# Optimization experiments

Hardware: AMD Instinct MI355X
Metric: run time of the kernel (lower is better)

## Reference

```python
import jax, jax.numpy as jnp
import numpy as np

B, LS, LW, D = 4, 160, 128, 768
POS_DIM = WD = PWD = DDD = 64
MAX_SPAN = 8
NZ = int(LW * 0.5)          # span_pruned_threshold = 0.5
HID = 128
SPAN_DIM = 2 * D + 2 * POS_DIM + WD      # 1728
PAIR_DIM = 2 * SPAN_DIM + PWD + DDD      # 3584
BINS = np.array([0, 1, 2, 3, 4, 5, 6, 7, 8, 9, 10, 15, 20, 25, 30, 50, 80])

def _span_indices(n, max_span):
    # enumeration order matches the torch loop: window = 1..max_span, start ascending
    s, e = [], []
    for w in range(1, min(n, max_span) + 1):
        st = np.arange(n - w + 1)
        s.append(st); e.append(st + w - 1)
    return np.concatenate(s), np.concatenate(e)

STARTS, ENDS = _span_indices(LW, MAX_SPAN)   # [S], S = 996
NUM_SPANS = len(STARTS)
WIDTH_IDS = np.searchsorted(BINS, ENDS - STARTS + 1, side='right') - 1  # bucket_embedding


def setup_inputs() -> dict:
    key = jax.random.key(0)
    ks = jax.random.split(key, 20)
    w = lambda k, shape, s=0.05: (jax.random.normal(k, shape, dtype=jnp.float32) * s)
    return {
        "last_hidden": jax.random.normal(ks[0], (B, LS, D), dtype=jnp.float32),
        "bert_subword_mask_matrix": jax.random.uniform(ks[1], (B, LS, LS), dtype=jnp.float32),
        "word_len": jnp.ones((B, LW), dtype=jnp.float32),
        "pos_table": w(ks[2], (50, POS_DIM), 1.0),
        "width_table": w(ks[3], (17, WD), 1.0),
        "rel_table": w(ks[4], (17, PWD), 1.0),
        "dep_table": w(ks[5], (30, DDD), 1.0),
        "sW1": w(ks[6], (SPAN_DIM, HID)), "sb1": jnp.zeros((HID,), jnp.float32),
        "sW2": w(ks[7], (HID, HID)),      "sb2": jnp.zeros((HID,), jnp.float32),
        "sW3": w(ks[8], (HID, 3)),        "sb3": jnp.zeros((3,), jnp.float32),
        "pW1": w(ks[9], (PAIR_DIM, HID)), "pb1": jnp.zeros((HID,), jnp.float32),
        "pW2": w(ks[10], (HID, HID)),     "pb2": jnp.zeros((HID,), jnp.float32),
        "pW3": w(ks[11], (HID, 4)),       "pb3": jnp.zeros((4,), jnp.float32),
        "first_subword_seq": jnp.sort(jax.random.randint(ks[12], (B, LW), 0, LS), axis=-1),
        "pos_id": jax.random.randint(ks[13], (B, LW), 0, 50),
        "dep_dis": jax.random.randint(ks[14], (B, LW, LW), 0, 30),
    }


def _ffnn(x, W1, b1, W2, b2, W3, b3):
    h = jax.nn.relu(x @ W1 + b1)
    h = jax.nn.relu(h @ W2 + b2)
    return h @ W3 + b3          # dropout is identity in eval mode


def reference(last_hidden, bert_subword_mask_matrix, word_len,
              pos_table, width_table, rel_table, dep_table,
              sW1, sb1, sW2, sb2, sW3, sb3,
              pW1, pb1, pW2, pb2, pW3, pb3,
              first_subword_seq, pos_id, dep_dis):
    # subword -> word features
    feats = jnp.einsum('bst,btd->bsd', bert_subword_mask_matrix, last_hidden)   # [B,LS,D]
    feats = jnp.take_along_axis(feats, first_subword_seq[:, :, None], axis=1)   # [B,LW,D]
    feats = feats / word_len[:, :, None]
    pos_feats = pos_table[pos_id]                                               # [B,LW,64]

    # span representation: [x_i; x_j; p_i; p_j; width_emb]
    w_emb = width_table[WIDTH_IDS]                                              # [S,64]
    spans = jnp.concatenate([
        feats[:, STARTS], feats[:, ENDS],
        pos_feats[:, STARTS], pos_feats[:, ENDS],
        jnp.broadcast_to(w_emb[None], (B, NUM_SPANS, WD))], axis=-1)            # [B,S,1728]

    span_prob = _ffnn(spans, sW1, sb1, sW2, sb2, sW3, sb3)                       # [B,S,3]

    # pruned target/opinion spans
    t_idx = jax.lax.top_k(span_prob[:, :, 1], NZ)[1]                             # [B,NZ]
    o_idx = jax.lax.top_k(span_prob[:, :, 2], NZ)[1]
    t_pair = jnp.repeat(t_idx, NZ, axis=1)                                       # itertools.product order
    o_pair = jnp.tile(o_idx, (1, NZ))                                            # [B,P], P = NZ*NZ

    starts = jnp.asarray(STARTS); ends = jnp.asarray(ENDS)
    a, b = starts[t_pair], ends[t_pair]
    c, d = starts[o_pair], ends[o_pair]

    # f_distance: min(|b-c|, |a-d|), bucketed
    rel = jnp.minimum(jnp.abs(b - c), jnp.abs(a - d))
    rel_ids = jnp.searchsorted(jnp.asarray(BINS), rel, side='right') - 1
    rel_emb = rel_table[rel_ids]                                                 # [B,P,64]

    # dep distance: min of dep_dis[a:b+1, c:d+1]
    BIG = jnp.int32(2 ** 30)
    dep_pad = jnp.pad(dep_dis.astype(jnp.int32),
                      ((0, 0), (0, MAX_SPAN), (0, MAX_SPAN)), constant_values=2 ** 30)
    r = jnp.arange(MAX_SPAN)

    def block_min(dm, ai, bi, ci, di):
        blk = jax.lax.dynamic_slice(dm, (ai, ci), (MAX_SPAN, MAX_SPAN))
        mask = (r[:, None] <= bi - ai) & (r[None, :] <= di - ci)
        return jnp.min(jnp.where(mask, blk, BIG))

    dep_ids = jax.vmap(jax.vmap(block_min, in_axes=(None, 0, 0, 0, 0)),
                       in_axes=(0, 0, 0, 0, 0))(dep_pad, a, b, c, d)             # [B,P]
    dep_emb = dep_table[dep_ids]                                                 # [B,P,64]

    span_t = jnp.take_along_axis(spans, t_pair[:, :, None], axis=1)              # [B,P,1728]
    span_o = jnp.take_along_axis(spans, o_pair[:, :, None], axis=1)
    pair_feat = jnp.concatenate([span_t, span_o, rel_emb, dep_emb], axis=-1)     # [B,P,3584]

    pair_prob = _ffnn(pair_feat, pW1, pb1, pW2, pb2, pW3, pb3)                   # [B,P,4]
    return span_prob, pair_prob
```

## Files before the change

### kernel.cpp

```cpp
#include <hip/hip_runtime.h>

#define BB 4
#define LS 160
#define LW 128
#define DD 768
#define NSPANS 996
#define NZv 64
#define NPAIR 4096
#define HID 128
#define XLD 832
#define PROJ_N 393216


__device__ inline void span_decode(int s, int& st, int& en, int& w) {
  int ww = 1, base = 0;
  while (ww < 8 && s >= base + (129 - ww)) { base += 129 - ww; ++ww; }
  st = s - base; en = st + ww - 1; w = ww;
}

__device__ inline int bucket17(int v) {
  const int BINSv[17] = {0,1,2,3,4,5,6,7,8,9,10,15,20,25,30,50,80};
  int r = 0;
#pragma unroll
  for (int k = 1; k < 17; ++k) r += (v >= BINSv[k]) ? 1 : 0;
  return r;
}

__global__ __launch_bounds__(256) void prep_kernel(
    const float* __restrict__ mask, const float* __restrict__ lh,
    const int* __restrict__ fss, const float* __restrict__ wlen,
    const int* __restrict__ pos_id, const float* __restrict__ pos_table,
    const float* __restrict__ width_table, const float* __restrict__ rel_table,
    const float* __restrict__ dep_table, const float* __restrict__ sW1,
    const float* __restrict__ pW1, const float* __restrict__ sb1,
    const float* __restrict__ pb1, float* __restrict__ X,
    float* __restrict__ tabs) {
  int gid = blockIdx.x;
  int tid = threadIdx.x;
  if (gid < 96) {
    int nt = gid % 12, mt = gid / 12;
    int b = mt >> 1;
    int row0 = mt * 64, c0 = nt * 64;
    __shared__ float as[16][68];
    __shared__ float bs[16][68];
    __shared__ int fssl[64];
    __shared__ float wll[64];
    if (tid < 64) { fssl[tid] = fss[row0 + tid]; wll[tid] = wlen[row0 + tid]; }
    __syncthreads();
    int rg = tid >> 4, tc = tid & 15;
    float acc[4][4] = {{0.f}};
    for (int k0 = 0; k0 < LS; k0 += 16) {
      {
        int r = tid >> 2, kb = (tid & 3) * 4;
        float4 mv = *(const float4*)(mask + (size_t)(b * LS + fssl[r]) * LS + k0 + kb);
        as[kb + 0][r] = mv.x; as[kb + 1][r] = mv.y;
        as[kb + 2][r] = mv.z; as[kb + 3][r] = mv.w;
      }
      {
        int c = tid & 63, kq = tid >> 6;
#pragma unroll
        for (int q = 0; q < 4; ++q) {
          int kk = kq * 4 + q;
          bs[kk][c] = lh[(size_t)(b * LS + k0 + kk) * DD + c0 + c];
        }
      }
      __syncthreads();
#pragma unroll
      for (int kk = 0; kk < 16; ++kk) {
        float av[4], bv[4];
#pragma unroll
        for (int i = 0; i < 4; ++i) av[i] = as[kk][rg * 4 + i];
#pragma unroll
        for (int j = 0; j < 4; ++j) bv[j] = bs[kk][tc * 4 + j];
#pragma unroll
        for (int i = 0; i < 4; ++i)
#pragma unroll
          for (int j = 0; j < 4; ++j) acc[i][j] += av[i] * bv[j];
      }
      __syncthreads();
    }
#pragma unroll
    for (int i = 0; i < 4; ++i) {
      int r = rg * 4 + i;
      float wl = wll[r];
      float4 v = make_float4(acc[i][0] / wl, acc[i][1] / wl, acc[i][2] / wl, acc[i][3] / wl);
      *(float4*)(X + (size_t)(row0 + r) * XLD + c0 + tc * 4) = v;
    }
  } else if (gid < 104) {
    int e0 = (gid - 96) * 4096 + tid * 16;
    int row = e0 >> 6, c0 = e0 & 63;
    const float* src = pos_table + pos_id[row] * 64 + c0;
    float* dst = X + (size_t)row * XLD + 768 + c0;
#pragma unroll
    for (int q = 0; q < 4; ++q)
      *(float4*)(dst + q * 4) = *(const float4*)(src + q * 4);
  } else {
    int bt = gid - 104;
    const float *src, *W, *bias; int rows; float* out;
    switch (bt) {
      case 0: src = width_table; W = sW1 + 1664 * HID; bias = sb1;    rows = 17; out = tabs;        break;
      case 1: src = width_table; W = pW1 + 1664 * HID; bias = nullptr; rows = 17; out = tabs + 2176; break;
      case 2: src = width_table; W = pW1 + 3392 * HID; bias = nullptr; rows = 17; out = tabs + 4352; break;
      case 3: src = rel_table;   W = pW1 + 3456 * HID; bias = nullptr; rows = 17; out = tabs + 6528; break;
      default:src = dep_table;   W = pW1 + 3520 * HID; bias = pb1;    rows = 30; out = tabs + 8704; break;
    }
    for (int e = tid; e < rows * HID; e += 256) {
      int r = e >> 7, c = e & 127;
      float acc = 0.f;
#pragma unroll 8
      for (int k = 0; k < 64; ++k) acc += src[r * 64 + k] * W[k * HID + c];
      out[e] = acc + (bias ? bias[c] : 0.f);
    }
  }
}

__global__ __launch_bounds__(256) void proj_gemm(
    const float* __restrict__ X, const float* __restrict__ sW1,
    const float* __restrict__ pW1, float* __restrict__ part) {
  int nt = blockIdx.x, mt = blockIdx.y, ks = blockIdx.z;
  const int f_offs[6] = {0, 768, 0, 768, 1728, 2496};
  const int p_offs[6] = {1536, 1600, 1536, 1600, 3264, 3328};
  int g = nt >> 1;
  const float* Wb = (g < 2) ? sW1 : pW1;
  int f_off = f_offs[g], p_off = p_offs[g];
  int c0 = (nt & 1) * 64;
  int row0 = mt * 64;
  int kbase = ks * 416;
  __shared__ float as[16][68];
  __shared__ float bs[16][68];
  int tid = threadIdx.x;
  int rg = tid >> 4, tc = tid & 15;
  float acc[4][4] = {{0.f}};
  for (int k0 = 0; k0 < 416; k0 += 16) {
    {
      int r = tid >> 2, kb = (tid & 3) * 4;
      float4 xv = *(const float4*)(X + (size_t)(row0 + r) * XLD + kbase + k0 + kb);
      as[kb + 0][r] = xv.x; as[kb + 1][r] = xv.y;
      as[kb + 2][r] = xv.z; as[kb + 3][r] = xv.w;
    }
    {
      int c = tid & 63, kq = tid >> 6;
#pragma unroll
      for (int q = 0; q < 4; ++q) {
        int kk = kq * 4 + q;
        int kg = kbase + k0 + kk;
        int wr = (kg < 768) ? (f_off + kg) : (p_off + kg - 768);
        bs[kk][c] = Wb[(size_t)wr * HID + c0 + c];
      }
    }
    __syncthreads();
#pragma unroll
    for (int kk = 0; kk < 16; ++kk) {
      float av[4], bv[4];
#pragma unroll
      for (int i = 0; i < 4; ++i) av[i] = as[kk][rg * 4 + i];
#pragma unroll
      for (int j = 0; j < 4; ++j) bv[j] = bs[kk][tc * 4 + j];
#pragma unroll
      for (int i = 0; i < 4; ++i)
#pragma unroll
        for (int j = 0; j < 4; ++j) acc[i][j] += av[i] * bv[j];
    }
    __syncthreads();
  }
#pragma unroll
  for (int i = 0; i < 4; ++i) {
    int row = row0 + rg * 4 + i;
    int bb = row >> 7, iloc = row & 127;
    float* dst = part + (size_t)ks * PROJ_N +
                 ((size_t)(g * BB + bb) * LW + iloc) * HID + c0 + tc * 4;
    *(float4*)dst = make_float4(acc[i][0], acc[i][1], acc[i][2], acc[i][3]);
  }
}

__global__ __launch_bounds__(256) void span_kernel(
    const float* __restrict__ part, const float* __restrict__ tabs,
    const float* __restrict__ sW2, const float* __restrict__ sb2,
    const float* __restrict__ sW3, const float* __restrict__ sb3,
    float* __restrict__ out) {
  int b = blockIdx.y, s0 = blockIdx.x * 32;
  int cnt = min(32, NSPANS - s0);
  __shared__ float h[32][129];
  __shared__ float wsh[16][132];
  __shared__ int stl[32], enl[32], wdl[32];
  int tid = threadIdx.x;
  if (tid < 32 && tid < cnt) {
    int st, en, w; span_decode(s0 + tid, st, en, w);
    stl[tid] = st; enl[tid] = en; wdl[tid] = w;
  }
  __syncthreads();
  const float* SA0 = part + (size_t)(0 * BB + b) * LW * HID;
  const float* SB0 = part + (size_t)(1 * BB + b) * LW * HID;
  const float* SA1 = SA0 + PROJ_N;
  const float* SB1 = SB0 + PROJ_N;
  const float* SW = tabs;
#pragma unroll
  for (int u = 0; u < 16; ++u) {
    int e = tid + u * 256; int r = e >> 7, c = e & 127;
    float v = 0.f;
    if (r < cnt) {
      int sa = stl[r] * HID + c, sb = enl[r] * HID + c;
      v = ((SA0[sa] + SA1[sa]) + (SB0[sb] + SB1[sb])) + SW[wdl[r] * HID + c];
    }
    h[r][c] = fmaxf(v, 0.f);
  }
  __syncthreads();
  int rg = tid >> 5, tc = tid & 31;
  float acc[4][4] = {{0.f}};
  for (int k0 = 0; k0 < HID; k0 += 16) {
#pragma unroll
    for (int u = 0; u < 8; ++u) {
      int idx = tid + u * 256; int r = idx >> 7, c = idx & 127;
      wsh[r][c] = sW2[(k0 + r) * HID + c];
    }
    __syncthreads();
#pragma unroll
    for (int kk = 0; kk < 16; ++kk) {
      float av[4], bv[4];
#pragma unroll
      for (int i = 0; i < 4; ++i) av[i] = h[rg * 4 + i][k0 + kk];
#pragma unroll
      for (int j = 0; j < 4; ++j) bv[j] = wsh[kk][tc * 4 + j];
#pragma unroll
      for (int i = 0; i < 4; ++i)
#pragma unroll
        for (int j = 0; j < 4; ++j) acc[i][j] += av[i] * bv[j];
    }
    __syncthreads();
  }
  __shared__ float h2[32][129];
#pragma unroll
  for (int i = 0; i < 4; ++i)
#pragma unroll
    for (int j = 0; j < 4; ++j)
      h2[rg * 4 + i][tc * 4 + j] = fmaxf(acc[i][j] + sb2[tc * 4 + j], 0.f);
  __syncthreads();
  if (tid < 96) {
    int sl = tid / 3, oc = tid - sl * 3;
    if (sl < cnt) {
      float a = sb3[oc];
#pragma unroll 16
      for (int k = 0; k < HID; ++k) a += h2[sl][k] * sW3[k * 3 + oc];
      out[(b * NSPANS + s0 + sl) * 3 + oc] = a;
    }
  }
}

__global__ __launch_bounds__(256) void topk_kernel(
    const float* __restrict__ out, int* __restrict__ tix, int* __restrict__ oix) {
  int b = blockIdx.y, ch = blockIdx.x + 1;
  __shared__ unsigned long long keys[1024];
  int tid = threadIdx.x;
#pragma unroll
  for (int u = 0; u < 4; ++u) {
    int e = tid + u * 256;
    unsigned long long kk = 0ull;
    if (e < NSPANS) {
      unsigned int bits = __float_as_uint(out[(b * NSPANS + e) * 3 + ch]);
      unsigned int mv = (bits & 0x80000000u) ? ~bits : (bits | 0x80000000u);
      kk = ((unsigned long long)mv << 32) | (unsigned long long)(0xFFFFFFFFu - e);
    }
    keys[e] = kk;
  }
  __syncthreads();
  for (int k = 2; k <= 1024; k <<= 1) {
    for (int j = k >> 1; j > 0; j >>= 1) {
#pragma unroll
      for (int u = 0; u < 4; ++u) {
        int i = tid + u * 256;
        int l = i ^ j;
        if (l > i) {
          unsigned long long a = keys[i], c = keys[l];
          bool desc = ((i & k) == 0);
          if (desc ? (a < c) : (a > c)) { keys[i] = c; keys[l] = a; }
        }
      }
      __syncthreads();
    }
  }
  int* dst = (ch == 1 ? tix : oix) + b * NZv;
  if (tid < NZv) dst[tid] = (int)(0xFFFFFFFFu - (unsigned int)keys[tid]);
}

__global__ __launch_bounds__(256) void pair_kernel(
    const float* __restrict__ part, const float* __restrict__ tabs,
    const int* __restrict__ tix, const int* __restrict__ oix,
    const int* __restrict__ dep_dis, const float* __restrict__ pW2,
    const float* __restrict__ pb2, const float* __restrict__ pW3,
    const float* __restrict__ pb3, float* __restrict__ out) {
  int b = blockIdx.y, p0 = blockIdx.x * 64;
  __shared__ float h[64][129];
  __shared__ float wsh[16][132];
  __shared__ int mTA[64], mTB[64], mOA[64], mOB[64], mTW[64], mOW[64], mR[64], mD[64];
  int tid = threadIdx.x;
  {
    int m = tid >> 2, sub = tid & 3;
    int p = p0 + m;
    int ti = tix[b * NZv + (p >> 6)];
    int oi = oix[b * NZv + (p & 63)];
    int a, bb2, wt, c, d, wo;
    span_decode(ti, a, bb2, wt);
    span_decode(oi, c, d, wo);
    int mn = 0x7FFFFFFF;
    const int* dp = dep_dis + b * LW * LW;
    for (int x = a; x <= bb2; ++x)
      for (int y = c + sub; y <= d; y += 4)
        mn = min(mn, dp[x * LW + y]);
    mn = min(mn, __shfl_xor(mn, 1));
    mn = min(mn, __shfl_xor(mn, 2));
    if (sub == 0) {
      int rel = min(abs(bb2 - c), abs(a - d));
      mTA[m] = ((2 * BB + b) * LW + a)   * HID;
      mTB[m] = ((3 * BB + b) * LW + bb2) * HID;
      mOA[m] = ((4 * BB + b) * LW + c)   * HID;
      mOB[m] = ((5 * BB + b) * LW + d)   * HID;
      mTW[m] = 2176 + wt * HID;
      mOW[m] = 4352 + wo * HID;
      mR[m]  = 6528 + bucket17(rel) * HID;
      mD[m]  = 8704 + mn * HID;
    }
  }
  __syncthreads();
#pragma unroll
  for (int u = 0; u < 32; ++u) {
    int e = tid + u * 256; int r = e >> 7, c = e & 127;
    int ta = mTA[r] + c, tb = mTB[r] + c, oa = mOA[r] + c, ob = mOB[r] + c;
    float v = (part[ta] + part[ta + PROJ_N]) + (part[tb] + part[tb + PROJ_N]) +
              (part[oa] + part[oa + PROJ_N]) + (part[ob] + part[ob + PROJ_N]) +
              tabs[mTW[r] + c] + tabs[mOW[r] + c] +
              tabs[mR[r] + c] + tabs[mD[r] + c];
    h[r][c] = fmaxf(v, 0.f);
  }
  __syncthreads();
  int tr = tid >> 5, tc = tid & 31;
  float acc[8][4] = {{0.f}};
  for (int k0 = 0; k0 < HID; k0 += 16) {
#pragma unroll
    for (int u = 0; u < 8; ++u) {
      int idx = tid + u * 256; int r = idx >> 7, c = idx & 127;
      wsh[r][c] = pW2[(k0 + r) * HID + c];
    }
    __syncthreads();
#pragma unroll
    for (int kk = 0; kk < 16; ++kk) {
      float av[8], bv[4];
#pragma unroll
      for (int i = 0; i < 8; ++i) av[i] = h[tr + 8 * i][k0 + kk];
#pragma unroll
      for (int j = 0; j < 4; ++j) bv[j] = wsh[kk][tc + 32 * j];
#pragma unroll
      for (int i = 0; i < 8; ++i)
#pragma unroll
        for (int j = 0; j < 4; ++j) acc[i][j] += av[i] * bv[j];
    }
    __syncthreads();
  }
#pragma unroll
  for (int i = 0; i < 8; ++i)
#pragma unroll
    for (int j = 0; j < 4; ++j)
      h[tr + 8 * i][tc + 32 * j] = fmaxf(acc[i][j] + pb2[tc + 32 * j], 0.f);
  __syncthreads();
  {
    int sl = tid >> 2, oc = tid & 3;
    float a = pb3[oc];
#pragma unroll 16
    for (int k = 0; k < HID; ++k) a += h[sl][k] * pW3[k * 4 + oc];
    out[BB * NSPANS * 3 + (b * NPAIR + p0 + sl) * 4 + oc] = a;
  }
}

extern "C" void kernel_launch(void* const* d_in, const int* in_sizes, int n_in,
                              void* d_out, int out_size, void* d_ws, size_t ws_size,
                              hipStream_t stream) {
  const float* last_hidden = (const float*)d_in[0];
  const float* mask        = (const float*)d_in[1];
  const float* word_len    = (const float*)d_in[2];
  const float* pos_table   = (const float*)d_in[3];
  const float* width_table = (const float*)d_in[4];
  const float* rel_table   = (const float*)d_in[5];
  const float* dep_table   = (const float*)d_in[6];
  const float* sW1 = (const float*)d_in[7];
  const float* sb1 = (const float*)d_in[8];
  const float* sW2 = (const float*)d_in[9];
  const float* sb2 = (const float*)d_in[10];
  const float* sW3 = (const float*)d_in[11];
  const float* sb3 = (const float*)d_in[12];
  const float* pW1 = (const float*)d_in[13];
  const float* pb1 = (const float*)d_in[14];
  const float* pW2 = (const float*)d_in[15];
  const float* pb2 = (const float*)d_in[16];
  const float* pW3 = (const float*)d_in[17];
  const float* pb3 = (const float*)d_in[18];
  const int* fss     = (const int*)d_in[19];
  const int* pos_id  = (const int*)d_in[20];
  const int* dep_dis = (const int*)d_in[21];

  float* ws   = (float*)d_ws;
  float* X    = ws;
  float* part = ws + 425984;
  float* tabs = ws + 1212416;
  int*   tix  = (int*)(ws + 1224960);
  int*   oix  = tix + 256;
  float* out  = (float*)d_out;

  prep_kernel<<<109, 256, 0, stream>>>(mask, last_hidden, fss, word_len,
                                       pos_id, pos_table, width_table, rel_table,
                                       dep_table, sW1, pW1, sb1, pb1, X, tabs);
  proj_gemm<<<dim3(12, 8, 2), 256, 0, stream>>>(X, sW1, pW1, part);
  span_kernel<<<dim3(32, BB), 256, 0, stream>>>(part, tabs, sW2, sb2, sW3, sb3, out);
  topk_kernel<<<dim3(2, BB), 256, 0, stream>>>(out, tix, oix);
  pair_kernel<<<dim3(64, BB), 256, 0, stream>>>(part, tabs, tix, oix, dep_dis,
                                                pW2, pb2, pW3, pb3, out);
}
```

Measured before the change: 222.1 us.

## Fuse five stage kernels into one cooperative persistent kernel with grid syncs

Merges prep, projection GEMM, span FFNN, top-k and pair FFNN into a single cooperative kernel of 256 blocks. Stages are separated by grid.sync() and share one union of shared-memory layouts. This removes four kernel launches and the gaps between them. In exchange, shared memory per block grows to the size of the largest stage, many blocks sit idle in the small stages, and each grid barrier has its own cost.

```diff
diff --git a/kernel.cpp b/kernel.cpp
--- a/kernel.cpp
+++ b/kernel.cpp
@@ -1,4 +1,7 @@
 #include <hip/hip_runtime.h>
+#include <hip/hip_cooperative_groups.h>
+
+namespace cg = cooperative_groups;
 
 #define BB 4
 #define LS 160
@@ -26,42 +29,56 @@
   return r;
 }
 
-__global__ __launch_bounds__(256) void prep_kernel(
+struct FeatsSM { float as[16][68]; float bs[16][68]; int fssl[64]; float wll[64]; };
+struct ProjSM  { float as[16][68]; float bs[16][68]; };
+struct SpanSM  { float h[32][129]; float h2[32][129]; float wsh[16][132];
+                 int stl[32], enl[32], wdl[32]; };
+struct TopkSM  { unsigned long long keys[1024]; };
+struct PairSM  { float h[64][129]; float wsh[16][132];
+                 int mTA[64], mTB[64], mOA[64], mOB[64],
+                     mTW[64], mOW[64], mR[64], mD[64]; };
+union AllSM { FeatsSM f; ProjSM p; SpanSM s; TopkSM t; PairSM q; };
+
+__global__ __launch_bounds__(256) void fused_kernel(
     const float* __restrict__ mask, const float* __restrict__ lh,
     const int* __restrict__ fss, const float* __restrict__ wlen,
     const int* __restrict__ pos_id, const float* __restrict__ pos_table,
     const float* __restrict__ width_table, const float* __restrict__ rel_table,
-    const float* __restrict__ dep_table, const float* __restrict__ sW1,
-    const float* __restrict__ pW1, const float* __restrict__ sb1,
-    const float* __restrict__ pb1, float* __restrict__ X,
-    float* __restrict__ tabs) {
-  int gid = blockIdx.x;
-  int tid = threadIdx.x;
+    const float* __restrict__ dep_table,
+    const float* __restrict__ sW1, const float* __restrict__ sb1,
+    const float* __restrict__ sW2, const float* __restrict__ sb2,
+    const float* __restrict__ sW3, const float* __restrict__ sb3,
+    const float* __restrict__ pW1, const float* __restrict__ pb1,
+    const float* __restrict__ pW2, const float* __restrict__ pb2,
+    const float* __restrict__ pW3, const float* __restrict__ pb3,
+    const int* __restrict__ dep_dis,
+    float* __restrict__ X, float* __restrict__ part, float* __restrict__ tabs,
+    int* __restrict__ tix, int* __restrict__ oix, float* __restrict__ out) {
+  cg::grid_group grid = cg::this_grid();
+  int gid = blockIdx.x, tid = threadIdx.x;
+  __shared__ __align__(16) AllSM sm;
+
   if (gid < 96) {
     int nt = gid % 12, mt = gid / 12;
     int b = mt >> 1;
     int row0 = mt * 64, c0 = nt * 64;
-    __shared__ float as[16][68];
-    __shared__ float bs[16][68];
-    __shared__ int fssl[64];
-    __shared__ float wll[64];
-    if (tid < 64) { fssl[tid] = fss[row0 + tid]; wll[tid] = wlen[row0 + tid]; }
+    if (tid < 64) { sm.f.fssl[tid] = fss[row0 + tid]; sm.f.wll[tid] = wlen[row0 + tid]; }
     __syncthreads();
     int rg = tid >> 4, tc = tid & 15;
     float acc[4][4] = {{0.f}};
     for (int k0 = 0; k0 < LS; k0 += 16) {
       {
         int r = tid >> 2, kb = (tid & 3) * 4;
-        float4 mv = *(const float4*)(mask + (size_t)(b * LS + fssl[r]) * LS + k0 + kb);
-        as[kb + 0][r] = mv.x; as[kb + 1][r] = mv.y;
-        as[kb + 2][r] = mv.z; as[kb + 3][r] = mv.w;
+        float4 mv = *(const float4*)(mask + (size_t)(b * LS + sm.f.fssl[r]) * LS + k0 + kb);
+        sm.f.as[kb + 0][r] = mv.x; sm.f.as[kb + 1][r] = mv.y;
+        sm.f.as[kb + 2][r] = mv.z; sm.f.as[kb + 3][r] = mv.w;
       }
       {
         int c = tid & 63, kq = tid >> 6;
 #pragma unroll
         for (int q = 0; q < 4; ++q) {
           int kk = kq * 4 + q;
-          bs[kk][c] = lh[(size_t)(b * LS + k0 + kk) * DD + c0 + c];
+          sm.f.bs[kk][c] = lh[(size_t)(b * LS + k0 + kk) * DD + c0 + c];
         }
       }
       __syncthreads();
@@ -69,9 +86,9 @@
       for (int kk = 0; kk < 16; ++kk) {
         float av[4], bv[4];
 #pragma unroll
-        for (int i = 0; i < 4; ++i) av[i] = as[kk][rg * 4 + i];
-#pragma unroll
-        for (int j = 0; j < 4; ++j) bv[j] = bs[kk][tc * 4 + j];
+        for (int i = 0; i < 4; ++i) av[i] = sm.f.as[kk][rg * 4 + i];
+#pragma unroll
+        for (int j = 0; j < 4; ++j) bv[j] = sm.f.bs[kk][tc * 4 + j];
 #pragma unroll
         for (int i = 0; i < 4; ++i)
 #pragma unroll
@@ -82,7 +99,7 @@
 #pragma unroll
     for (int i = 0; i < 4; ++i) {
       int r = rg * 4 + i;
-      float wl = wll[r];
+      float wl = sm.f.wll[r];
       float4 v = make_float4(acc[i][0] / wl, acc[i][1] / wl, acc[i][2] / wl, acc[i][3] / wl);
       *(float4*)(X + (size_t)(row0 + r) * XLD + c0 + tc * 4) = v;
     }
@@ -94,292 +111,271 @@
 #pragma unroll
     for (int q = 0; q < 4; ++q)
       *(float4*)(dst + q * 4) = *(const float4*)(src + q * 4);
-  } else {
+  } else if (gid < 109) {
     int bt = gid - 104;
-    const float *src, *W, *bias; int rows; float* out;
+    const float *src, *W, *bias; int rows; float* o;
     switch (bt) {
-      case 0: src = width_table; W = sW1 + 1664 * HID; bias = sb1;    rows = 17; out = tabs;        break;
-      case 1: src = width_table; W = pW1 + 1664 * HID; bias = nullptr; rows = 17; out = tabs + 2176; break;
-      case 2: src = width_table; W = pW1 + 3392 * HID; bias = nullptr; rows = 17; out = tabs + 4352; break;
-      case 3: src = rel_table;   W = pW1 + 3456 * HID; bias = nullptr; rows = 17; out = tabs + 6528; break;
-      default:src = dep_table;   W = pW1 + 3520 * HID; bias = pb1;    rows = 30; out = tabs + 8704; break;
+      case 0: src = width_table; W = sW1 + 1664 * HID; bias = sb1;    rows = 17; o = tabs;        break;
+      case 1: src = width_table; W = pW1 + 1664 * HID; bias = nullptr; rows = 17; o = tabs + 2176; break;
+      case 2: src = width_table; W = pW1 + 3392 * HID; bias = nullptr; rows = 17; o = tabs + 4352; break;
+      case 3: src = rel_table;   W = pW1 + 3456 * HID; bias = nullptr; rows = 17; o = tabs + 6528; break;
+      default:src = dep_table;   W = pW1 + 3520 * HID; bias = pb1;    rows = 30; o = tabs + 8704; break;
     }
     for (int e = tid; e < rows * HID; e += 256) {
       int r = e >> 7, c = e & 127;
       float acc = 0.f;
 #pragma unroll 8
       for (int k = 0; k < 64; ++k) acc += src[r * 64 + k] * W[k * HID + c];
-      out[e] = acc + (bias ? bias[c] : 0.f);
+      o[e] = acc + (bias ? bias[c] : 0.f);
     }
   }
-}
-
-__global__ __launch_bounds__(256) void proj_gemm(
-    const float* __restrict__ X, const float* __restrict__ sW1,
-    const float* __restrict__ pW1, float* __restrict__ part) {
-  int nt = blockIdx.x, mt = blockIdx.y, ks = blockIdx.z;
-  const int f_offs[6] = {0, 768, 0, 768, 1728, 2496};
-  const int p_offs[6] = {1536, 1600, 1536, 1600, 3264, 3328};
-  int g = nt >> 1;
-  const float* Wb = (g < 2) ? sW1 : pW1;
-  int f_off = f_offs[g], p_off = p_offs[g];
-  int c0 = (nt & 1) * 64;
-  int row0 = mt * 64;
-  int kbase = ks * 416;
-  __shared__ float as[16][68];
-  __shared__ float bs[16][68];
-  int tid = threadIdx.x;
-  int rg = tid >> 4, tc = tid & 15;
-  float acc[4][4] = {{0.f}};
-  for (int k0 = 0; k0 < 416; k0 += 16) {
+  grid.sync();
+
+  if (gid < 192) {
+    int nt = gid % 12, mt = (gid / 12) % 8, ks = gid / 96;
+    const int f_offs[6] = {0, 768, 0, 768, 1728, 2496};
+    const int p_offs[6] = {1536, 1600, 1536, 1600, 3264, 3328};
+    int g = nt >> 1;
+    const float* Wb = (g < 2) ? sW1 : pW1;
+    int f_off = f_offs[g], p_off = p_offs[g];
+    int c0 = (nt & 1) * 64;
+    int row0 = mt * 64;
+    int kbase = ks * 416;
+    int rg = tid >> 4, tc = tid & 15;
+    float acc[4][4] = {{0.f}};
+    for (int k0 = 0; k0 < 416; k0 += 16) {
+      {
+        int r = tid >> 2, kb = (tid & 3) * 4;
+        float4 xv = *(const float4*)(X + (size_t)(row0 + r) * XLD + kbase + k0 + kb);
+        sm.p.as[kb + 0][r] = xv.x; sm.p.as[kb + 1][r] = xv.y;
+        sm.p.as[kb + 2][r] = xv.z; sm.p.as[kb + 3][r] = xv.w;
+      }
+      {
+        int c = tid & 63, kq = tid >> 6;
+#pragma unroll
+        for (int q = 0; q < 4; ++q) {
+          int kk = kq * 4 + q;
+          int kg = kbase + k0 + kk;
+          int wr = (kg < 768) ? (f_off + kg) : (p_off + kg - 768);
+          sm.p.bs[kk][c] = Wb[(size_t)wr * HID + c0 + c];
+        }
+      }
+      __syncthreads();
+#pragma unroll
+      for (int kk = 0; kk < 16; ++kk) {
+        float av[4], bv[4];
+#pragma unroll
+        for (int i = 0; i < 4; ++i) av[i] = sm.p.as[kk][rg * 4 + i];
+#pragma unroll
+        for (int j = 0; j < 4; ++j) bv[j] = sm.p.bs[kk][tc * 4 + j];
+#pragma unroll
+        for (int i = 0; i < 4; ++i)
+#pragma unroll
+          for (int j = 0; j < 4; ++j) acc[i][j] += av[i] * bv[j];
+      }
+      __syncthreads();
+    }
+#pragma unroll
+    for (int i = 0; i < 4; ++i) {
+      int row = row0 + rg * 4 + i;
+      int bb = row >> 7, iloc = row & 127;
+      float* dst = part + (size_t)ks * PROJ_N +
+                   ((size_t)(g * BB + bb) * LW + iloc) * HID + c0 + tc * 4;
+      *(float4*)dst = make_float4(acc[i][0], acc[i][1], acc[i][2], acc[i][3]);
+    }
+  }
+  grid.sync();
+
+  if (gid < 128) {
+    int b = gid >> 5, s0 = (gid & 31) * 32;
+    int cnt = min(32, NSPANS - s0);
+    if (tid < 32 && tid < cnt) {
+      int st, en, w; span_decode(s0 + tid, st, en, w);
+      sm.s.stl[tid] = st; sm.s.enl[tid] = en; sm.s.wdl[tid] = w;
+    }
+    __syncthreads();
+    const float* SA0 = part + (size_t)(0 * BB + b) * LW * HID;
+    const float* SB0 = part + (size_t)(1 * BB + b) * LW * HID;
+    const float* SA1 = SA0 + PROJ_N;
+    const float* SB1 = SB0 + PROJ_N;
+    const float* SW = tabs;
+#pragma unroll
+    for (int u = 0; u < 16; ++u) {
+      int e = tid + u * 256; int r = e >> 7, c = e & 127;
+      float v = 0.f;
+      if (r < cnt) {
+        int sa = sm.s.stl[r] * HID + c, sb = sm.s.enl[r] * HID + c;
+        v = ((SA0[sa] + SA1[sa]) + (SB0[sb] + SB1[sb])) + SW[sm.s.wdl[r] * HID + c];
+      }
+      sm.s.h[r][c] = fmaxf(v, 0.f);
+    }
+    __syncthreads();
+    int rg = tid >> 5, tc = tid & 31;
+    float acc[4][4] = {{0.f}};
+    for (int k0 = 0; k0 < HID; k0 += 16) {
+#pragma unroll
+      for (int u = 0; u < 8; ++u) {
+        int idx = tid + u * 256; int r = idx >> 7, c = idx & 127;
+        sm.s.wsh[r][c] = sW2[(k0 + r) * HID + c];
+      }
+      __syncthreads();
+#pragma unroll
+      for (int kk = 0; kk < 16; ++kk) {
+        float av[4], bv[4];
+#pragma unroll
+        for (int i = 0; i < 4; ++i) av[i] = sm.s.h[rg * 4 + i][k0 + kk];
+#pragma unroll
+        for (int j = 0; j < 4; ++j) bv[j] = sm.s.wsh[kk][tc * 4 + j];
+#pragma unroll
+        for (int i = 0; i < 4; ++i)
+#pragma unroll
+          for (int j = 0; j < 4; ++j) acc[i][j] += av[i] * bv[j];
+      }
+      __syncthreads();
+    }
+#pragma unroll
+    for (int i = 0; i < 4; ++i)
+#pragma unroll
+      for (int j = 0; j < 4; ++j)
+        sm.s.h2[rg * 4 + i][tc * 4 + j] = fmaxf(acc[i][j] + sb2[tc * 4 + j], 0.f);
+    __syncthreads();
+    if (tid < 96) {
+      int sl = tid / 3, oc = tid - sl * 3;
+      if (sl < cnt) {
+        float a = sb3[oc];
+#pragma unroll 16
+        for (int k = 0; k < HID; ++k) a += sm.s.h2[sl][k] * sW3[k * 3 + oc];
+        out[(b * NSPANS + s0 + sl) * 3 + oc] = a;
+      }
+    }
+  }
+  grid.sync();
+
+  if (gid < 8) {
+    int b = gid >> 1, ch = (gid & 1) + 1;
+#pragma unroll
+    for (int u = 0; u < 4; ++u) {
+      int e = tid + u * 256;
+      unsigned long long kk = 0ull;
+      if (e < NSPANS) {
+        unsigned int bits = __float_as_uint(out[(b * NSPANS + e) * 3 + ch]);
+        unsigned int mv = (bits & 0x80000000u) ? ~bits : (bits | 0x80000000u);
+        kk = ((unsigned long long)mv << 32) | (unsigned long long)(0xFFFFFFFFu - e);
+      }
+      sm.t.keys[e] = kk;
+    }
+    __syncthreads();
+    for (int k = 2; k <= 1024; k <<= 1) {
+      for (int j = k >> 1; j > 0; j >>= 1) {
+#pragma unroll
+        for (int u = 0; u < 4; ++u) {
+          int i = tid + u * 256;
+          int l = i ^ j;
+          if (l > i) {
+            unsigned long long a = sm.t.keys[i], c = sm.t.keys[l];
+            bool desc = ((i & k) == 0);
+            if (desc ? (a < c) : (a > c)) { sm.t.keys[i] = c; sm.t.keys[l] = a; }
+          }
+        }
+        __syncthreads();
+      }
+    }
+    int* dst = (ch == 1 ? tix : oix) + b * NZv;
+    if (tid < NZv) dst[tid] = (int)(0xFFFFFFFFu - (unsigned int)sm.t.keys[tid]);
+  }
+  grid.sync();
+
+  {
+    int b = gid >> 6, p0 = (gid & 63) * 64;
     {
-      int r = tid >> 2, kb = (tid & 3) * 4;
-      float4 xv = *(const float4*)(X + (size_t)(row0 + r) * XLD + kbase + k0 + kb);
-      as[kb + 0][r] = xv.x; as[kb + 1][r] = xv.y;
-      as[kb + 2][r] = xv.z; as[kb + 3][r] = xv.w;
-    }
+      int m = tid >> 2, sub = tid & 3;
+      int p = p0 + m;
+      int ti = tix[b * NZv + (p >> 6)];
+      int oi = oix[b * NZv + (p & 63)];
+      int a, bb2, wt, c, d, wo;
+      span_decode(ti, a, bb2, wt);
+      span_decode(oi, c, d, wo);
+      int mn = 0x7FFFFFFF;
+      const int* dp = dep_dis + b * LW * LW;
+      for (int x = a; x <= bb2; ++x)
+        for (int y = c + sub; y <= d; y += 4)
+          mn = min(mn, dp[x * LW + y]);
+      mn = min(mn, __shfl_xor(mn, 1));
+      mn = min(mn, __shfl_xor(mn, 2));
+      if (sub == 0) {
+        int rel = min(abs(bb2 - c), abs(a - d));
+        sm.q.mTA[m] = ((2 * BB + b) * LW + a)   * HID;
+        sm.q.mTB[m] = ((3 * BB + b) * LW + bb2) * HID;
+        sm.q.mOA[m] = ((4 * BB + b) * LW + c)   * HID;
+        sm.q.mOB[m] = ((5 * BB + b) * LW + d)   * HID;
+        sm.q.mTW[m] = 2176 + wt * HID;
+        sm.q.mOW[m] = 4352 + wo * HID;
+        sm.q.mR[m]  = 6528 + bucket17(rel) * HID;
+        sm.q.mD[m]  = 8704 + mn * HID;
+      }
+    }
+    __syncthreads();
+#pragma unroll
+    for (int u = 0; u < 32; ++u) {
+      int e = tid + u * 256; int r = e >> 7, c = e & 127;
+      int ta = sm.q.mTA[r] + c, tb = sm.q.mTB[r] + c;
+      int oa = sm.q.mOA[r] + c, ob = sm.q.mOB[r] + c;
+      float v = (part[ta] + part[ta + PROJ_N]) + (part[tb] + part[tb + PROJ_N]) +
+                (part[oa] + part[oa + PROJ_N]) + (part[ob] + part[ob + PROJ_N]) +
+                tabs[sm.q.mTW[r] + c] + tabs[sm.q.mOW[r] + c] +
+                tabs[sm.q.mR[r] + c] + tabs[sm.q.mD[r] + c];
+      sm.q.h[r][c] = fmaxf(v, 0.f);
+    }
+    __syncthreads();
+    int tr = tid >> 5, tc = tid & 31;
+    float acc[8][4] = {{0.f}};
+    for (int k0 = 0; k0 < HID; k0 += 16) {
+#pragma unroll
+      for (int u = 0; u < 8; ++u) {
+        int idx = tid + u * 256; int r = idx >> 7, c = idx & 127;
+        sm.q.wsh[r][c] = pW2[(k0 + r) * HID + c];
+      }
+      __syncthreads();
+#pragma unroll
+      for (int kk = 0; kk < 16; ++kk) {
+        float av[8], bv[4];
+#pragma unroll
+        for (int i = 0; i < 8; ++i) av[i] = sm.q.h[tr + 8 * i][k0 + kk];
+#pragma unroll
+        for (int j = 0; j < 4; ++j) bv[j] = sm.q.wsh[kk][tc + 32 * j];
+#pragma unroll
+        for (int i = 0; i < 8; ++i)
+#pragma unroll
+          for (int j = 0; j < 4; ++j) acc[i][j] += av[i] * bv[j];
+      }
+      __syncthreads();
+    }
+#pragma unroll
+    for (int i = 0; i < 8; ++i)
+#pragma unroll
+      for (int j = 0; j < 4; ++j)
+        sm.q.h[tr + 8 * i][tc + 32 * j] = fmaxf(acc[i][j] + pb2[tc + 32 * j], 0.f);
+    __syncthreads();
     {
-      int c = tid & 63, kq = tid >> 6;
-#pragma unroll
-      for (int q = 0; q < 4; ++q) {
-        int kk = kq * 4 + q;
-        int kg = kbase + k0 + kk;
-        int wr = (kg < 768) ? (f_off + kg) : (p_off + kg - 768);
-        bs[kk][c] = Wb[(size_t)wr * HID + c0 + c];
-      }
-    }
-    __syncthreads();
-#pragma unroll
-    for (int kk = 0; kk < 16; ++kk) {
-      float av[4], bv[4];
-#pragma unroll
-      for (int i = 0; i < 4; ++i) av[i] = as[kk][rg * 4 + i];
-#pragma unroll
-      for (int j = 0; j < 4; ++j) bv[j] = bs[kk][tc * 4 + j];
-#pragma unroll
-      for (int i = 0; i < 4; ++i)
-#pragma unroll
-        for (int j = 0; j < 4; ++j) acc[i][j] += av[i] * bv[j];
-    }
-    __syncthreads();
-  }
-#pragma unroll
-  for (int i = 0; i < 4; ++i) {
-    int row = row0 + rg * 4 + i;
-    int bb = row >> 7, iloc = row & 127;
-    float* dst = part + (size_t)ks * PROJ_N +
-                 ((size_t)(g * BB + bb) * LW + iloc) * HID + c0 + tc * 4;
-    *(float4*)dst = make_float4(acc[i][0], acc[i][1], acc[i][2], acc[i][3]);
-  }
-}
-
-__global__ __launch_bounds__(256) void span_kernel(
-    const float* __restrict__ part, const float* __restrict__ tabs,
-    const float* __restrict__ sW2, const float* __restrict__ sb2,
-    const float* __restrict__ sW3, const float* __restrict__ sb3,
-    float* __restrict__ out) {
-  int b = blockIdx.y, s0 = blockIdx.x * 32;
-  int cnt = min(32, NSPANS - s0);
-  __shared__ float h[32][129];
-  __shared__ float wsh[16][132];
-  __shared__ int stl[32], enl[32], wdl[32];
-  int tid = threadIdx.x;
-  if (tid < 32 && tid < cnt) {
-    int st, en, w; span_decode(s0 + tid, st, en, w);
-    stl[tid] = st; enl[tid] = en; wdl[tid] = w;
-  }
-  __syncthreads();
-  const float* SA0 = part + (size_t)(0 * BB + b) * LW * HID;
-  const float* SB0 = part + (size_t)(1 * BB + b) * LW * HID;
-  const float* SA1 = SA0 + PROJ_N;
-  const float* SB1 = SB0 + PROJ_N;
-  const float* SW = tabs;
-#pragma unroll
-  for (int u = 0; u < 16; ++u) {
-    int e = tid + u * 256; int r = e >> 7, c = e & 127;
-    float v = 0.f;
-    if (r < cnt) {
-      int sa = stl[r] * HID + c, sb = enl[r] * HID + c;
-      v = ((SA0[sa] + SA1[sa]) + (SB0[sb] + SB1[sb])) + SW[wdl[r] * HID + c];
-    }
-    h[r][c] = fmaxf(v, 0.f);
-  }
-  __syncthreads();
-  int rg = tid >> 5, tc = tid & 31;
-  float acc[4][4] = {{0.f}};
-  for (int k0 = 0; k0 < HID; k0 += 16) {
-#pragma unroll
-    for (int u = 0; u < 8; ++u) {
-      int idx = tid + u * 256; int r = idx >> 7, c = idx & 127;
-      wsh[r][c] = sW2[(k0 + r) * HID + c];
-    }
-    __syncthreads();
-#pragma unroll
-    for (int kk = 0; kk < 16; ++kk) {
-      float av[4], bv[4];
-#pragma unroll
-      for (int i = 0; i < 4; ++i) av[i] = h[rg * 4 + i][k0 + kk];
-#pragma unroll
-      for (int j = 0; j < 4; ++j) bv[j] = wsh[kk][tc * 4 + j];
-#pragma unroll
-      for (int i = 0; i < 4; ++i)
-#pragma unroll
-        for (int j = 0; j < 4; ++j) acc[i][j] += av[i] * bv[j];
-    }
-    __syncthreads();
-  }
-  __shared__ float h2[32][129];
-#pragma unroll
-  for (int i = 0; i < 4; ++i)
-#pragma unroll
-    for (int j = 0; j < 4; ++j)
-      h2[rg * 4 + i][tc * 4 + j] = fmaxf(acc[i][j] + sb2[tc * 4 + j], 0.f);
-  __syncthreads();
-  if (tid < 96) {
-    int sl = tid / 3, oc = tid - sl * 3;
-    if (sl < cnt) {
-      float a = sb3[oc];
+      int sl = tid >> 2, oc = tid & 3;
+      float a = pb3[oc];
 #pragma unroll 16
-      for (int k = 0; k < HID; ++k) a += h2[sl][k] * sW3[k * 3 + oc];
-      out[(b * NSPANS + s0 + sl) * 3 + oc] = a;
-    }
-  }
-}
-
-__global__ __launch_bounds__(256) void topk_kernel(
-    const float* __restrict__ out, int* __restrict__ tix, int* __restrict__ oix) {
-  int b = blockIdx.y, ch = blockIdx.x + 1;
-  __shared__ unsigned long long keys[1024];
-  int tid = threadIdx.x;
-#pragma unroll
-  for (int u = 0; u < 4; ++u) {
-    int e = tid + u * 256;
-    unsigned long long kk = 0ull;
-    if (e < NSPANS) {
-      unsigned int bits = __float_as_uint(out[(b * NSPANS + e) * 3 + ch]);
-      unsigned int mv = (bits & 0x80000000u) ? ~bits : (bits | 0x80000000u);
-      kk = ((unsigned long long)mv << 32) | (unsigned long long)(0xFFFFFFFFu - e);
-    }
-    keys[e] = kk;
-  }
-  __syncthreads();
-  for (int k = 2; k <= 1024; k <<= 1) {
-    for (int j = k >> 1; j > 0; j >>= 1) {
-#pragma unroll
-      for (int u = 0; u < 4; ++u) {
-        int i = tid + u * 256;
-        int l = i ^ j;
-        if (l > i) {
-          unsigned long long a = keys[i], c = keys[l];
-          bool desc = ((i & k) == 0);
-          if (desc ? (a < c) : (a > c)) { keys[i] = c; keys[l] = a; }
-        }
-      }
-      __syncthreads();
-    }
-  }
-  int* dst = (ch == 1 ? tix : oix) + b * NZv;
-  if (tid < NZv) dst[tid] = (int)(0xFFFFFFFFu - (unsigned int)keys[tid]);
-}
-
-__global__ __launch_bounds__(256) void pair_kernel(
-    const float* __restrict__ part, const float* __restrict__ tabs,
-    const int* __restrict__ tix, const int* __restrict__ oix,
-    const int* __restrict__ dep_dis, const float* __restrict__ pW2,
-    const float* __restrict__ pb2, const float* __restrict__ pW3,
-    const float* __restrict__ pb3, float* __restrict__ out) {
-  int b = blockIdx.y, p0 = blockIdx.x * 64;
-  __shared__ float h[64][129];
-  __shared__ float wsh[16][132];
-  __shared__ int mTA[64], mTB[64], mOA[64], mOB[64], mTW[64], mOW[64], mR[64], mD[64];
-  int tid = threadIdx.x;
-  {
-    int m = tid >> 2, sub = tid & 3;
-    int p = p0 + m;
-    int ti = tix[b * NZv + (p >> 6)];
-    int oi = oix[b * NZv + (p & 63)];
-    int a, bb2, wt, c, d, wo;
-    span_decode(ti, a, bb2, wt);
-    span_decode(oi, c, d, wo);
-    int mn = 0x7FFFFFFF;
-    const int* dp = dep_dis + b * LW * LW;
-    for (int x = a; x <= bb2; ++x)
-      for (int y = c + sub; y <= d; y += 4)
-        mn = min(mn, dp[x * LW + y]);
-    mn = min(mn, __shfl_xor(mn, 1));
-    mn = min(mn, __shfl_xor(mn, 2));
-    if (sub == 0) {
-      int rel = min(abs(bb2 - c), abs(a - d));
-      mTA[m] = ((2 * BB + b) * LW + a)   * HID;
-      mTB[m] = ((3 * BB + b) * LW + bb2) * HID;
-      mOA[m] = ((4 * BB + b) * LW + c)   * HID;
-      mOB[m] = ((5 * BB + b) * LW + d)   * HID;
-      mTW[m] = 2176 + wt * HID;
-      mOW[m] = 4352 + wo * HID;
-      mR[m]  = 6528 + bucket17(rel) * HID;
-      mD[m]  = 8704 + mn * HID;
-    }
-  }
-  __syncthreads();
-#pragma unroll
-  for (int u = 0; u < 32; ++u) {
-    int e = tid + u * 256; int r = e >> 7, c = e & 127;
-    int ta = mTA[r] + c, tb = mTB[r] + c, oa = mOA[r] + c, ob = mOB[r] + c;
-    float v = (part[ta] + part[ta + PROJ_N]) + (part[tb] + part[tb + PROJ_N]) +
-              (part[oa] + part[oa + PROJ_N]) + (part[ob] + part[ob + PROJ_N]) +
-              tabs[mTW[r] + c] + tabs[mOW[r] + c] +
-              tabs[mR[r] + c] + tabs[mD[r] + c];
-    h[r][c] = fmaxf(v, 0.f);
-  }
-  __syncthreads();
-  int tr = tid >> 5, tc = tid & 31;
-  float acc[8][4] = {{0.f}};
-  for (int k0 = 0; k0 < HID; k0 += 16) {
-#pragma unroll
-    for (int u = 0; u < 8; ++u) {
-      int idx = tid + u * 256; int r = idx >> 7, c = idx & 127;
-      wsh[r][c] = pW2[(k0 + r) * HID + c];
-    }
-    __syncthreads();
-#pragma unroll
-    for (int kk = 0; kk < 16; ++kk) {
-      float av[8], bv[4];
-#pragma unroll
-      for (int i = 0; i < 8; ++i) av[i] = h[tr + 8 * i][k0 + kk];
-#pragma unroll
-      for (int j = 0; j < 4; ++j) bv[j] = wsh[kk][tc + 32 * j];
-#pragma unroll
-      for (int i = 0; i < 8; ++i)
-#pragma unroll
-        for (int j = 0; j < 4; ++j) acc[i][j] += av[i] * bv[j];
-    }
-    __syncthreads();
-  }
-#pragma unroll
-  for (int i = 0; i < 8; ++i)
-#pragma unroll
-    for (int j = 0; j < 4; ++j)
-      h[tr + 8 * i][tc + 32 * j] = fmaxf(acc[i][j] + pb2[tc + 32 * j], 0.f);
-  __syncthreads();
-  {
-    int sl = tid >> 2, oc = tid & 3;
-    float a = pb3[oc];
-#pragma unroll 16
-    for (int k = 0; k < HID; ++k) a += h[sl][k] * pW3[k * 4 + oc];
-    out[BB * NSPANS * 3 + (b * NPAIR + p0 + sl) * 4 + oc] = a;
+      for (int k = 0; k < HID; ++k) a += sm.q.h[sl][k] * pW3[k * 4 + oc];
+      out[BB * NSPANS * 3 + (b * NPAIR + p0 + sl) * 4 + oc] = a;
+    }
   }
 }
 
 extern "C" void kernel_launch(void* const* d_in, const int* in_sizes, int n_in,
                               void* d_out, int out_size, void* d_ws, size_t ws_size,
                               hipStream_t stream) {
-  const float* last_hidden = (const float*)d_in[0];
-  const float* mask        = (const float*)d_in[1];
-  const float* word_len    = (const float*)d_in[2];
-  const float* pos_table   = (const float*)d_in[3];
-  const float* width_table = (const float*)d_in[4];
-  const float* rel_table   = (const float*)d_in[5];
-  const float* dep_table   = (const float*)d_in[6];
+  const float* mask_p      = (const float*)d_in[1];
+  const float* lh_p        = (const float*)d_in[0];
+  const float* wlen_p      = (const float*)d_in[2];
+  const float* pos_table_p = (const float*)d_in[3];
+  const float* width_p     = (const float*)d_in[4];
+  const float* rel_p       = (const float*)d_in[5];
+  const float* dep_p       = (const float*)d_in[6];
   const float* sW1 = (const float*)d_in[7];
   const float* sb1 = (const float*)d_in[8];
   const float* sW2 = (const float*)d_in[9];
@@ -392,9 +388,9 @@
   const float* pb2 = (const float*)d_in[16];
   const float* pW3 = (const float*)d_in[17];
   const float* pb3 = (const float*)d_in[18];
-  const int* fss     = (const int*)d_in[19];
-  const int* pos_id  = (const int*)d_in[20];
-  const int* dep_dis = (const int*)d_in[21];
+  const int* fss_p     = (const int*)d_in[19];
+  const int* pos_id_p  = (const int*)d_in[20];
+  const int* dep_dis_p = (const int*)d_in[21];
 
   float* ws   = (float*)d_ws;
   float* X    = ws;
@@ -402,14 +398,17 @@
   float* tabs = ws + 1212416;
   int*   tix  = (int*)(ws + 1224960);
   int*   oix  = tix + 256;
-  float* out  = (float*)d_out;
-
-  prep_kernel<<<109, 256, 0, stream>>>(mask, last_hidden, fss, word_len,
-                                       pos_id, pos_table, width_table, rel_table,
-                                       dep_table, sW1, pW1, sb1, pb1, X, tabs);
-  proj_gemm<<<dim3(12, 8, 2), 256, 0, stream>>>(X, sW1, pW1, part);
-  span_kernel<<<dim3(32, BB), 256, 0, stream>>>(part, tabs, sW2, sb2, sW3, sb3, out);
-  topk_kernel<<<dim3(2, BB), 256, 0, stream>>>(out, tix, oix);
-  pair_kernel<<<dim3(64, BB), 256, 0, stream>>>(part, tabs, tix, oix, dep_dis,
-                                                pW2, pb2, pW3, pb3, out);
+  float* outp = (float*)d_out;
+
+  void* args[] = {
+    (void*)&mask_p, (void*)&lh_p, (void*)&fss_p, (void*)&wlen_p,
+    (void*)&pos_id_p, (void*)&pos_table_p, (void*)&width_p, (void*)&rel_p,
+    (void*)&dep_p,
+    (void*)&sW1, (void*)&sb1, (void*)&sW2, (void*)&sb2, (void*)&sW3, (void*)&sb3,
+    (void*)&pW1, (void*)&pb1, (void*)&pW2, (void*)&pb2, (void*)&pW3, (void*)&pb3,
+    (void*)&dep_dis_p,
+    (void*)&X, (void*)&part, (void*)&tabs, (void*)&tix, (void*)&oix, (void*)&outp
+  };
+  hipLaunchCooperativeKernel((void*)fused_kernel, dim3(256), dim3(256),
+                             args, 0, stream);
 }
```

New measurement: 361.1 us. 62.5% more time.
